# Kernel tuning notes

Hardware: AMD Instinct MI355X
Metric: run time of the kernel (lower is better)

Reference implementation:

```python
import jax, jax.numpy as jnp
import numpy as np

INPUT_DIM = 784
LATENT_DIM = 32
HIDDEN = 256
NUM_PROTO = 25  # 5x5 SOM grid
BATCH = 65536


def setup_inputs() -> dict:
    key = jax.random.key(0)
    ks = jax.random.split(key, 10)
    s = lambda fan_in: 1.0 / np.sqrt(fan_in)
    return {
        "x": jax.random.uniform(ks[0], (BATCH, INPUT_DIM), dtype=jnp.float32),
        # encoder: Linear(784,256) -> ReLU -> Linear(256,32)
        "We1": jax.random.normal(ks[1], (INPUT_DIM, HIDDEN), dtype=jnp.float32) * s(INPUT_DIM),
        "be1": jnp.zeros((HIDDEN,), dtype=jnp.float32),
        "We2": jax.random.normal(ks[2], (HIDDEN, LATENT_DIM), dtype=jnp.float32) * s(HIDDEN),
        "be2": jnp.zeros((LATENT_DIM,), dtype=jnp.float32),
        # decoder: Linear(32,256) -> ReLU -> Linear(256,784) -> Sigmoid
        "Wd1": jax.random.normal(ks[3], (LATENT_DIM, HIDDEN), dtype=jnp.float32) * s(LATENT_DIM),
        "bd1": jnp.zeros((HIDDEN,), dtype=jnp.float32),
        "Wd2": jax.random.normal(ks[4], (HIDDEN, INPUT_DIM), dtype=jnp.float32) * s(HIDDEN),
        "bd2": jnp.zeros((INPUT_DIM,), dtype=jnp.float32),
        # SOM prototypes (torch.randn init)
        "prototypes": jax.random.normal(ks[5], (NUM_PROTO, LATENT_DIM), dtype=jnp.float32),
    }


def reference(x, We1, be1, We2, be2, Wd1, bd1, Wd2, bd2, prototypes):
    # encoder
    h = jax.nn.relu(x @ We1 + be1)          # [B, 256]
    z = h @ We2 + be2                        # [B, 32]
    # SOM layer: cdist -> argmin -> gather winning prototype
    # squared euclidean distance suffices for argmin
    sq_dists = (jnp.sum(z * z, axis=1, keepdims=True)
                - 2.0 * (z @ prototypes.T)
                + jnp.sum(prototypes * prototypes, axis=1))  # [B, 25]
    min_idx = jnp.argmin(sq_dists, axis=1)   # [B]
    som_z = prototypes[min_idx]              # [B, 32]
    # decoder
    hd = jax.nn.relu(som_z @ Wd1 + bd1)      # [B, 256]
    x_recon = jax.nn.sigmoid(hd @ Wd2 + bd2)  # [B, 784]
    return (x_recon, z, som_z)
```

## Files before the change

kernel.cpp:

```cpp
#include <hip/hip_runtime.h>
#include <hip/hip_bf16.h>
#include <math.h>

#define BATCH   65536
#define IN_DIM  784
#define HID     256
#define LAT     32
#define NPROTO  25

typedef short  short8  __attribute__((ext_vector_type(8)));
typedef float  floatx4 __attribute__((ext_vector_type(4)));

__device__ __forceinline__ unsigned short f2bf(float v) {
    __hip_bfloat16 b = __float2bfloat16(v);
    return *reinterpret_cast<unsigned short*>(&b);
}
__device__ __forceinline__ float bf2f(unsigned short u) {
    __hip_bfloat16 b = *reinterpret_cast<__hip_bfloat16*>(&u);
    return __bfloat162float(b);
}
__device__ __forceinline__ void split3(float v, unsigned short& o1,
                                       unsigned short& o2, unsigned short& o3) {
    o1 = f2bf(v); float r1 = v - bf2f(o1);
    o2 = f2bf(r1); float r2 = r1 - bf2f(o2);
    o3 = f2bf(r2);
}

__device__ __forceinline__ floatx4 mm_bf16(short8 a, short8 b, floatx4 c) {
    return __builtin_amdgcn_mfma_f32_16x16x32_bf16(a, b, c, 0, 0, 0);
}

__device__ __forceinline__ void async_copy16(const void* g, void* l) {
    __builtin_amdgcn_global_load_lds(
        (const __attribute__((address_space(1))) unsigned int*)g,
        (__attribute__((address_space(3))) unsigned int*)l, 16, 0, 0);
}

#define BT_BYTES   409600
#define WS_NEEDED  1307200

__global__ __launch_bounds__(256)
void dpsom_prep(const float* __restrict__ We1,
                unsigned short* __restrict__ B1,
                unsigned short* __restrict__ B2,
                unsigned short* __restrict__ B3,
                const float* __restrict__ protos,
                const float* __restrict__ Wd1,
                const float* __restrict__ bd1,
                const float* __restrict__ Wd2,
                const float* __restrict__ bd2,
                float* __restrict__ table)
{
    const int tid = threadIdx.x;
    if (blockIdx.x < 200) {
        int e = (blockIdx.x * 256 + tid) * 4;
        int k = e & 31;
        int n = (e >> 5) & 255;
        int s = e >> 13;
        int cs = (k >> 3) ^ ((n >> 1) & 3);
        int dst = (s * 256 + n) * 32 + cs * 8 + (k & 7);
        ushort4 u1, u2, u3;
        unsigned short a, b, c;
#pragma unroll
        for (int j = 0; j < 4; ++j) {
            int kk = s * 32 + k + j;
            float v = (kk < IN_DIM) ? We1[(size_t)kk * HID + n] : 0.f;
            split3(v, a, b, c);
            ((unsigned short*)&u1)[j] = a;
            ((unsigned short*)&u2)[j] = b;
            ((unsigned short*)&u3)[j] = c;
        }
        *(ushort4*)(B1 + dst) = u1;
        *(ushort4*)(B2 + dst) = u2;
        *(ushort4*)(B3 + dst) = u3;
    } else {
        __shared__ float pr[LAT];
        __shared__ float hd[HID];
        const int p = blockIdx.x - 200;
        if (tid < LAT) pr[tid] = protos[p * LAT + tid];
        __syncthreads();
        float s = bd1[tid];
#pragma unroll
        for (int k = 0; k < LAT; ++k)
            s = fmaf(pr[k], Wd1[k * HID + tid], s);
        hd[tid] = fmaxf(s, 0.f);
        __syncthreads();
        for (int i = tid; i < IN_DIM; i += 256) {
            float o = bd2[i];
            for (int j = 0; j < HID; ++j)
                o = fmaf(hd[j], Wd2[(size_t)j * IN_DIM + i], o);
            table[p * IN_DIM + i] = 1.f / (1.f + expf(-o));
        }
    }
}

__global__ __launch_bounds__(256, 2)
void dpsom_encoder_mfma(const float* __restrict__ x,
                        const unsigned short* __restrict__ B1g,
                        const unsigned short* __restrict__ B2g,
                        const unsigned short* __restrict__ B3g,
                        const float* __restrict__ be1,
                        const float* __restrict__ We2,
                        const float* __restrict__ be2,
                        const float* __restrict__ protos,
                        const float* __restrict__ table,
                        float* __restrict__ z_out,
                        float* __restrict__ somz_out,
                        float* __restrict__ xrec)
{
    __shared__ __align__(16) char smem[61440];
    const int tid  = threadIdx.x;
    const int wave = tid >> 6;
    const int lane = tid & 63;
    const int l15  = lane & 15;
    const int q    = lane >> 4;
    const int sw   = (l15 >> 1) & 3;
    const int row0 = blockIdx.x * 64;

    floatx4 acc[4][4];
#pragma unroll
    for (int i = 0; i < 4; ++i)
#pragma unroll
        for (int j = 0; j < 4; ++j) acc[i][j] = (floatx4)0.f;

    int row_[2], k4_[2], dst_[2];
    const float* xptr[2];
#pragma unroll
    for (int i = 0; i < 2; ++i) {
        int ff = tid + i * 256;
        row_[i] = ff >> 3;
        k4_[i]  = ff & 7;
        int csw = ((k4_[i] >> 1) ^ ((row_[i] >> 1) & 3));
        dst_[i] = row_[i] * 64 + csw * 16 + (k4_[i] & 1) * 8;
        xptr[i] = x + (size_t)(row0 + row_[i]) * IN_DIM + k4_[i] * 4;
    }

    float4 cur[2], nxt[2];
#pragma unroll
    for (int i = 0; i < 2; ++i) cur[i] = *(const float4*)(xptr[i]);

    for (int s = 0; s < 25; ++s) {
        __syncthreads();
        if (s < 24) {
#pragma unroll
            for (int i = 0; i < 2; ++i) {
                nxt[i] = make_float4(0.f, 0.f, 0.f, 0.f);
                if (s + 1 < 24 || k4_[i] < 4)
                    nxt[i] = *(const float4*)(xptr[i] + (s + 1) * 32);
            }
        }
        {
            size_t gbase = (size_t)s * 16384 + (size_t)wave * 4096 + (size_t)lane * 16;
            char* lb = smem + 12288 + wave * 4096 + lane * 16;
#pragma unroll
            for (int i = 0; i < 4; ++i) {
                async_copy16((const char*)B1g + gbase + i * 1024, lb + 0     + i * 1024);
                async_copy16((const char*)B2g + gbase + i * 1024, lb + 16384 + i * 1024);
                async_copy16((const char*)B3g + gbase + i * 1024, lb + 32768 + i * 1024);
            }
        }
#pragma unroll
        for (int i = 0; i < 2; ++i) {
            float4 v = cur[i];
            ushort4 u1, u2, u3;
            unsigned short a, b, c;
            split3(v.x, a, b, c); u1.x = a; u2.x = b; u3.x = c;
            split3(v.y, a, b, c); u1.y = a; u2.y = b; u3.y = c;
            split3(v.z, a, b, c); u1.z = a; u2.z = b; u3.z = c;
            split3(v.w, a, b, c); u1.w = a; u2.w = b; u3.w = c;
            *(ushort4*)(smem + dst_[i])        = u1;
            *(ushort4*)(smem + 4096 + dst_[i]) = u2;
            *(ushort4*)(smem + 8192 + dst_[i]) = u3;
        }
        __syncthreads();

        short8 afr[3][4];
#pragma unroll
        for (int mf = 0; mf < 4; ++mf) {
            int abyte = (16 * mf + l15) * 64 + ((q ^ sw) * 16);
            afr[0][mf] = *(short8*)(smem + abyte);
            afr[1][mf] = *(short8*)(smem + 4096 + abyte);
            afr[2][mf] = *(short8*)(smem + 8192 + abyte);
        }
#pragma unroll
        for (int nf = 0; nf < 4; ++nf) {
            int n = wave * 64 + 16 * nf + l15;
            int bbyte = n * 64 + ((q ^ sw) * 16);
            short8 b1 = *(short8*)(smem + 12288 + bbyte);
            short8 b2 = *(short8*)(smem + 28672 + bbyte);
            short8 b3 = *(short8*)(smem + 45056 + bbyte);
#pragma unroll
            for (int mf = 0; mf < 4; ++mf) {
                floatx4 t = acc[mf][nf];
                t = mm_bf16(afr[0][mf], b1, t);
                t = mm_bf16(afr[0][mf], b2, t);
                t = mm_bf16(afr[1][mf], b1, t);
                t = mm_bf16(afr[1][mf], b2, t);
                t = mm_bf16(afr[0][mf], b3, t);
                t = mm_bf16(afr[2][mf], b1, t);
                acc[mf][nf] = t;
            }
        }
#pragma unroll
        for (int i = 0; i < 2; ++i) cur[i] = nxt[i];
    }

    {
        float bias[4];
#pragma unroll
        for (int nf = 0; nf < 4; ++nf) bias[nf] = be1[wave * 64 + 16 * nf + l15];
#pragma unroll
        for (int mf = 0; mf < 4; ++mf)
#pragma unroll
            for (int nf = 0; nf < 4; ++nf)
#pragma unroll
                for (int r = 0; r < 4; ++r)
                    acc[mf][nf][r] = fmaxf(acc[mf][nf][r] + bias[nf], 0.f);
    }

    float* h_lds = (float*)smem;
    float* z_lds = (float*)(smem + 33280);
    int*  minidx = (int*)(smem + 41728);

    const int jz = tid & 31;
    const int rg = tid >> 5;
    const float bz = be2[jz];

    for (int half = 0; half < 2; ++half) {
        __syncthreads();
#pragma unroll
        for (int mm = 0; mm < 2; ++mm) {
            int mf = 2 * half + mm;
#pragma unroll
            for (int nf = 0; nf < 4; ++nf)
#pragma unroll
                for (int r = 0; r < 4; ++r) {
                    int lr = 16 * mm + 4 * q + r;
                    h_lds[lr * 260 + wave * 64 + 16 * nf + l15] = acc[mf][nf][r];
                }
        }
        __syncthreads();
        float s0 = bz, s1 = bz, s2 = bz, s3 = bz;
        const float* h0p = h_lds + (rg * 4 + 0) * 260;
        const float* h1p = h_lds + (rg * 4 + 1) * 260;
        const float* h2p = h_lds + (rg * 4 + 2) * 260;
        const float* h3p = h_lds + (rg * 4 + 3) * 260;
#pragma unroll 4
        for (int c = 0; c < HID; c += 4) {
            float w0 = We2[(c + 0) * LAT + jz];
            float w1 = We2[(c + 1) * LAT + jz];
            float w2 = We2[(c + 2) * LAT + jz];
            float w3 = We2[(c + 3) * LAT + jz];
            float4 h0 = *(const float4*)(h0p + c);
            float4 h1 = *(const float4*)(h1p + c);
            float4 h2 = *(const float4*)(h2p + c);
            float4 h3 = *(const float4*)(h3p + c);
            s0 = fmaf(h0.x, w0, fmaf(h0.y, w1, fmaf(h0.z, w2, fmaf(h0.w, w3, s0))));
            s1 = fmaf(h1.x, w0, fmaf(h1.y, w1, fmaf(h1.z, w2, fmaf(h1.w, w3, s1))));
            s2 = fmaf(h2.x, w0, fmaf(h2.y, w1, fmaf(h2.z, w2, fmaf(h2.w, w3, s2))));
            s3 = fmaf(h3.x, w0, fmaf(h3.y, w1, fmaf(h3.z, w2, fmaf(h3.w, w3, s3))));
        }
        int rbase = half * 32 + rg * 4;
        z_lds[(rbase + 0) * 33 + jz] = s0;
        z_lds[(rbase + 1) * 33 + jz] = s1;
        z_lds[(rbase + 2) * 33 + jz] = s2;
        z_lds[(rbase + 3) * 33 + jz] = s3;
        z_out[(size_t)(row0 + rbase + 0) * LAT + jz] = s0;
        z_out[(size_t)(row0 + rbase + 1) * LAT + jz] = s1;
        z_out[(size_t)(row0 + rbase + 2) * LAT + jz] = s2;
        z_out[(size_t)(row0 + rbase + 3) * LAT + jz] = s3;
    }
    __syncthreads();

    if (tid < 64) {
        float zr[LAT];
        float zn = 0.f;
#pragma unroll
        for (int j = 0; j < LAT; ++j) {
            zr[j] = z_lds[tid * 33 + j];
            zn = fmaf(zr[j], zr[j], zn);
        }
        float best = 3.4e38f;
        int bp = 0;
        for (int p = 0; p < NPROTO; ++p) {
            float dot = 0.f, pn = 0.f;
#pragma unroll
            for (int j = 0; j < LAT; ++j) {
                float pv = protos[p * LAT + j];
                dot = fmaf(zr[j], pv, dot);
                pn  = fmaf(pv, pv, pn);
            }
            float d = zn - 2.f * dot + pn;
            if (d < best) { best = d; bp = p; }
        }
        minidx[tid] = bp;
    }
    __syncthreads();

#pragma unroll
    for (int m = 0; m < 8; ++m) {
        int r = rg * 8 + m;
        somz_out[(size_t)(row0 + r) * LAT + jz] = protos[minidx[r] * LAT + jz];
    }

    for (int i2 = tid; i2 < 64 * 196; i2 += 256) {
        int row = i2 / 196;
        int c   = i2 - row * 196;
        int idx = minidx[row];
        ((float4*)xrec)[(size_t)(row0 + row) * 196 + c] =
            ((const float4*)table)[idx * 196 + c];
    }
}

#define BMf 64
#define BKf 16
#define HSTRIDE 260
#define ZSTRIDE 33
#define SMEM_FLOATS 10432

__global__ __launch_bounds__(256)
void dpsom_encoder_fp32(const float* __restrict__ x,
                        const float* __restrict__ We1,
                        const float* __restrict__ be1,
                        const float* __restrict__ We2,
                        const float* __restrict__ be2,
                        const float* __restrict__ protos,
                        float* __restrict__ z_out,
                        float* __restrict__ somz_out,
                        int* __restrict__ minidx_out)
{
    __shared__ float smem[SMEM_FLOATS];
    __shared__ int minidx_lds[BMf];
    float* As = smem;
    float* Bs = smem + BKf * BMf;
    float* h_lds = smem;
    float* z_lds = smem + 32 * HSTRIDE;

    const int tid = threadIdx.x;
    const int tx = tid & 31;
    const int ty = tid >> 5;
    const int row0 = blockIdx.x * BMf;

    float acc[8][8];
#pragma unroll
    for (int i = 0; i < 8; ++i)
#pragma unroll
        for (int j = 0; j < 8; ++j) acc[i][j] = 0.f;

    const int ar  = tid >> 2;
    const int akq = tid & 3;

    for (int k0 = 0; k0 < IN_DIM; k0 += BKf) {
        __syncthreads();
        float4 av = *(const float4*)(x + (size_t)(row0 + ar) * IN_DIM + k0 + akq * 4);
        As[(akq * 4 + 0) * BMf + ar] = av.x;
        As[(akq * 4 + 1) * BMf + ar] = av.y;
        As[(akq * 4 + 2) * BMf + ar] = av.z;
        As[(akq * 4 + 3) * BMf + ar] = av.w;
#pragma unroll
        for (int i = 0; i < 4; ++i) {
            int f  = tid + i * 256;
            int bk = f >> 6;
            int bn = (f & 63) << 2;
            *(float4*)(Bs + bk * HID + bn) =
                *(const float4*)(We1 + (size_t)(k0 + bk) * HID + bn);
        }
        __syncthreads();
#pragma unroll
        for (int kk = 0; kk < BKf; ++kk) {
            float4 a0 = *(const float4*)(As + kk * BMf + ty * 8);
            float4 a1 = *(const float4*)(As + kk * BMf + ty * 8 + 4);
            float4 b0 = *(const float4*)(Bs + kk * HID + tx * 8);
            float4 b1 = *(const float4*)(Bs + kk * HID + tx * 8 + 4);
            float a[8] = {a0.x, a0.y, a0.z, a0.w, a1.x, a1.y, a1.z, a1.w};
            float b[8] = {b0.x, b0.y, b0.z, b0.w, b1.x, b1.y, b1.z, b1.w};
#pragma unroll
            for (int i = 0; i < 8; ++i)
#pragma unroll
                for (int j = 0; j < 8; ++j)
                    acc[i][j] = fmaf(a[i], b[j], acc[i][j]);
        }
    }
    {
        float bias[8];
#pragma unroll
        for (int j = 0; j < 8; ++j) bias[j] = be1[tx * 8 + j];
#pragma unroll
        for (int i = 0; i < 8; ++i)
#pragma unroll
            for (int j = 0; j < 8; ++j)
                acc[i][j] = fmaxf(acc[i][j] + bias[j], 0.f);
    }
    const int jz = tid & 31;
    const int rg = tid >> 5;
    const float bz = be2[jz];
    for (int half = 0; half < 2; ++half) {
        __syncthreads();
        if ((ty >> 2) == half) {
            int rb = (ty & 3) * 8;
#pragma unroll
            for (int i = 0; i < 8; ++i) {
                *(float4*)(h_lds + (rb + i) * HSTRIDE + tx * 8) =
                    make_float4(acc[i][0], acc[i][1], acc[i][2], acc[i][3]);
                *(float4*)(h_lds + (rb + i) * HSTRIDE + tx * 8 + 4) =
                    make_float4(acc[i][4], acc[i][5], acc[i][6], acc[i][7]);
            }
        }
        __syncthreads();
        float s0 = bz, s1 = bz, s2 = bz, s3 = bz;
        const float* h0p = h_lds + (rg * 4 + 0) * HSTRIDE;
        const float* h1p = h_lds + (rg * 4 + 1) * HSTRIDE;
        const float* h2p = h_lds + (rg * 4 + 2) * HSTRIDE;
        const float* h3p = h_lds + (rg * 4 + 3) * HSTRIDE;
#pragma unroll 4
        for (int c = 0; c < HID; c += 4) {
            float w0 = We2[(c + 0) * LAT + jz];
            float w1 = We2[(c + 1) * LAT + jz];
            float w2 = We2[(c + 2) * LAT + jz];
            float w3 = We2[(c + 3) * LAT + jz];
            float4 h0 = *(const float4*)(h0p + c);
            float4 h1 = *(const float4*)(h1p + c);
            float4 h2 = *(const float4*)(h2p + c);
            float4 h3 = *(const float4*)(h3p + c);
            s0 = fmaf(h0.x, w0, fmaf(h0.y, w1, fmaf(h0.z, w2, fmaf(h0.w, w3, s0))));
            s1 = fmaf(h1.x, w0, fmaf(h1.y, w1, fmaf(h1.z, w2, fmaf(h1.w, w3, s1))));
            s2 = fmaf(h2.x, w0, fmaf(h2.y, w1, fmaf(h2.z, w2, fmaf(h2.w, w3, s2))));
            s3 = fmaf(h3.x, w0, fmaf(h3.y, w1, fmaf(h3.z, w2, fmaf(h3.w, w3, s3))));
        }
        int rbase = half * 32 + rg * 4;
        z_lds[(rbase + 0) * ZSTRIDE + jz] = s0;
        z_lds[(rbase + 1) * ZSTRIDE + jz] = s1;
        z_lds[(rbase + 2) * ZSTRIDE + jz] = s2;
        z_lds[(rbase + 3) * ZSTRIDE + jz] = s3;
        z_out[(size_t)(row0 + rbase + 0) * LAT + jz] = s0;
        z_out[(size_t)(row0 + rbase + 1) * LAT + jz] = s1;
        z_out[(size_t)(row0 + rbase + 2) * LAT + jz] = s2;
        z_out[(size_t)(row0 + rbase + 3) * LAT + jz] = s3;
    }
    __syncthreads();
    if (tid < BMf) {
        float zr[LAT];
        float zn = 0.f;
#pragma unroll
        for (int j = 0; j < LAT; ++j) {
            zr[j] = z_lds[tid * ZSTRIDE + j];
            zn = fmaf(zr[j], zr[j], zn);
        }
        float best = 3.4e38f;
        int bp = 0;
        for (int p = 0; p < NPROTO; ++p) {
            float dot = 0.f, pn = 0.f;
#pragma unroll
            for (int j = 0; j < LAT; ++j) {
                float pv = protos[p * LAT + j];
                dot = fmaf(zr[j], pv, dot);
                pn  = fmaf(pv, pv, pn);
            }
            float d = zn - 2.f * dot + pn;
            if (d < best) { best = d; bp = p; }
        }
        minidx_out[row0 + tid] = bp;
        minidx_lds[tid] = bp;
    }
    __syncthreads();
#pragma unroll
    for (int m = 0; m < 8; ++m) {
        int r = rg * 8 + m;
        somz_out[(size_t)(row0 + r) * LAT + jz] = protos[minidx_lds[r] * LAT + jz];
    }
}

__global__ __launch_bounds__(256)
void dpsom_dectab(const float* __restrict__ protos,
                  const float* __restrict__ Wd1,
                  const float* __restrict__ bd1,
                  const float* __restrict__ Wd2,
                  const float* __restrict__ bd2,
                  float* __restrict__ table)
{
    __shared__ float pr[LAT];
    __shared__ float hd[HID];
    const int p = blockIdx.x;
    const int tid = threadIdx.x;
    if (tid < LAT) pr[tid] = protos[p * LAT + tid];
    __syncthreads();
    float s = bd1[tid];
#pragma unroll
    for (int k = 0; k < LAT; ++k)
        s = fmaf(pr[k], Wd1[k * HID + tid], s);
    hd[tid] = fmaxf(s, 0.f);
    __syncthreads();
    for (int i = tid; i < IN_DIM; i += 256) {
        float o = bd2[i];
        for (int j = 0; j < HID; ++j)
            o = fmaf(hd[j], Wd2[(size_t)j * IN_DIM + i], o);
        table[p * IN_DIM + i] = 1.f / (1.f + expf(-o));
    }
}

__global__ __launch_bounds__(256)
void dpsom_gather(const float4* __restrict__ table,
                  const int* __restrict__ minidx,
                  float4* __restrict__ xrec)
{
    const int f = blockIdx.x * 256 + threadIdx.x;
    const int row = f / 196;
    const int c4  = f - row * 196;
    const int idx = minidx[row];
    xrec[f] = table[idx * 196 + c4];
}

extern "C" void kernel_launch(void* const* d_in, const int* in_sizes, int n_in,
                              void* d_out, int out_size, void* d_ws, size_t ws_size,
                              hipStream_t stream)
{
    const float* x    = (const float*)d_in[0];
    const float* We1  = (const float*)d_in[1];
    const float* be1  = (const float*)d_in[2];
    const float* We2  = (const float*)d_in[3];
    const float* be2  = (const float*)d_in[4];
    const float* Wd1  = (const float*)d_in[5];
    const float* bd1  = (const float*)d_in[6];
    const float* Wd2  = (const float*)d_in[7];
    const float* bd2  = (const float*)d_in[8];
    const float* prot = (const float*)d_in[9];

    float* out   = (float*)d_out;
    float* xrec  = out;
    float* z_out = out + (size_t)BATCH * IN_DIM;
    float* somz  = z_out + (size_t)BATCH * LAT;

    if (ws_size >= WS_NEEDED) {
        unsigned short* B1 = (unsigned short*)d_ws;
        unsigned short* B2 = (unsigned short*)((char*)d_ws + BT_BYTES);
        unsigned short* B3 = (unsigned short*)((char*)d_ws + 2 * BT_BYTES);
        float* table = (float*)((char*)d_ws + 3 * BT_BYTES);

        hipLaunchKernelGGL(dpsom_prep, dim3(225), dim3(256), 0, stream,
                           We1, B1, B2, B3, prot, Wd1, bd1, Wd2, bd2, table);
        hipLaunchKernelGGL(dpsom_encoder_mfma, dim3(BATCH / 64), dim3(256), 0, stream,
                           x, B1, B2, B3, be1, We2, be2, prot, table,
                           z_out, somz, xrec);
    } else {
        int*   minidx = (int*)d_ws;
        float* table  = (float*)((char*)d_ws + (size_t)BATCH * 4);
        hipLaunchKernelGGL(dpsom_encoder_fp32, dim3(BATCH / BMf), dim3(256), 0, stream,
                           x, We1, be1, We2, be2, prot, z_out, somz, minidx);
        hipLaunchKernelGGL(dpsom_dectab, dim3(NPROTO), dim3(256), 0, stream,
                           prot, Wd1, bd1, Wd2, bd2, table);
        hipLaunchKernelGGL(dpsom_gather, dim3((BATCH * (IN_DIM / 4)) / 256), dim3(256), 0, stream,
                           (const float4*)table, minidx, (float4*)xrec);
    }
}
```

Measured before the change: 547.4 us.

## Load encoder weight fragments directly from global and double-buffer x tiles in LDS

Removes the async global-to-LDS staging of the three bf16 weight splits: each wave now loads its B fragments straight from global memory into registers, and the prep kernel drops the LDS swizzle. The x tile is double-buffered in LDS, so each step needs one barrier instead of two, and the split/store for the next step runs after the MFMAs. LDS use falls from about 60KB to about 41KB, which may allow more resident blocks. The cost is that every block re-reads the weights from global/L2 with non-coalesced per-lane 16-byte loads, and these loads are issued just before the MFMAs that use them, which could stall.

```diff
diff --git a/kernel.cpp b/kernel.cpp
--- a/kernel.cpp
+++ b/kernel.cpp
@@ -28,12 +28,6 @@
 
 __device__ __forceinline__ floatx4 mm_bf16(short8 a, short8 b, floatx4 c) {
     return __builtin_amdgcn_mfma_f32_16x16x32_bf16(a, b, c, 0, 0, 0);
-}
-
-__device__ __forceinline__ void async_copy16(const void* g, void* l) {
-    __builtin_amdgcn_global_load_lds(
-        (const __attribute__((address_space(1))) unsigned int*)g,
-        (__attribute__((address_space(3))) unsigned int*)l, 16, 0, 0);
 }
 
 #define BT_BYTES   409600
@@ -57,8 +51,7 @@
         int k = e & 31;
         int n = (e >> 5) & 255;
         int s = e >> 13;
-        int cs = (k >> 3) ^ ((n >> 1) & 3);
-        int dst = (s * 256 + n) * 32 + cs * 8 + (k & 7);
+        int dst = (s * 256 + n) * 32 + k;
         ushort4 u1, u2, u3;
         unsigned short a, b, c;
 #pragma unroll
@@ -108,7 +101,7 @@
                         float* __restrict__ somz_out,
                         float* __restrict__ xrec)
 {
-    __shared__ __align__(16) char smem[61440];
+    __shared__ __align__(16) char smem[41984];
     const int tid  = threadIdx.x;
     const int wave = tid >> 6;
     const int lane = tid & 63;
@@ -123,86 +116,96 @@
 #pragma unroll
         for (int j = 0; j < 4; ++j) acc[i][j] = (floatx4)0.f;
 
-    int row_[2], k4_[2], dst_[2];
+    int k4_[2], dst_[2];
     const float* xptr[2];
 #pragma unroll
     for (int i = 0; i < 2; ++i) {
         int ff = tid + i * 256;
-        row_[i] = ff >> 3;
+        int row = ff >> 3;
         k4_[i]  = ff & 7;
-        int csw = ((k4_[i] >> 1) ^ ((row_[i] >> 1) & 3));
-        dst_[i] = row_[i] * 64 + csw * 16 + (k4_[i] & 1) * 8;
-        xptr[i] = x + (size_t)(row0 + row_[i]) * IN_DIM + k4_[i] * 4;
-    }
-
-    float4 cur[2], nxt[2];
-#pragma unroll
-    for (int i = 0; i < 2; ++i) cur[i] = *(const float4*)(xptr[i]);
+        int csw = ((k4_[i] >> 1) ^ ((row >> 1) & 3));
+        dst_[i] = row * 64 + csw * 16 + (k4_[i] & 1) * 8;
+        xptr[i] = x + (size_t)(row0 + row) * IN_DIM + k4_[i] * 4;
+    }
+
+#pragma unroll
+    for (int i = 0; i < 2; ++i) {
+        float4 v = *(const float4*)(xptr[i]);
+        ushort4 u1, u2, u3;
+        unsigned short a, b, c;
+        split3(v.x, a, b, c); u1.x = a; u2.x = b; u3.x = c;
+        split3(v.y, a, b, c); u1.y = a; u2.y = b; u3.y = c;
+        split3(v.z, a, b, c); u1.z = a; u2.z = b; u3.z = c;
+        split3(v.w, a, b, c); u1.w = a; u2.w = b; u3.w = c;
+        *(ushort4*)(smem + dst_[i])        = u1;
+        *(ushort4*)(smem + 4096 + dst_[i]) = u2;
+        *(ushort4*)(smem + 8192 + dst_[i]) = u3;
+    }
+    __syncthreads();
 
     for (int s = 0; s < 25; ++s) {
-        __syncthreads();
+        const int cb = (s & 1) * 12288;
+        const int nb = ((s + 1) & 1) * 12288;
+
+        short8 bf1[4], bf2[4], bf3[4];
+#pragma unroll
+        for (int nf = 0; nf < 4; ++nf) {
+            size_t off = ((size_t)(s * 256 + wave * 64 + nf * 16 + l15)) * 32 + q * 8;
+            bf1[nf] = *(const short8*)(B1g + off);
+            bf2[nf] = *(const short8*)(B2g + off);
+            bf3[nf] = *(const short8*)(B3g + off);
+        }
+
+        float4 xv[2];
         if (s < 24) {
 #pragma unroll
             for (int i = 0; i < 2; ++i) {
-                nxt[i] = make_float4(0.f, 0.f, 0.f, 0.f);
+                xv[i] = make_float4(0.f, 0.f, 0.f, 0.f);
                 if (s + 1 < 24 || k4_[i] < 4)
-                    nxt[i] = *(const float4*)(xptr[i] + (s + 1) * 32);
+                    xv[i] = *(const float4*)(xptr[i] + (s + 1) * 32);
             }
         }
-        {
-            size_t gbase = (size_t)s * 16384 + (size_t)wave * 4096 + (size_t)lane * 16;
-            char* lb = smem + 12288 + wave * 4096 + lane * 16;
-#pragma unroll
-            for (int i = 0; i < 4; ++i) {
-                async_copy16((const char*)B1g + gbase + i * 1024, lb + 0     + i * 1024);
-                async_copy16((const char*)B2g + gbase + i * 1024, lb + 16384 + i * 1024);
-                async_copy16((const char*)B3g + gbase + i * 1024, lb + 32768 + i * 1024);
-            }
-        }
-#pragma unroll
-        for (int i = 0; i < 2; ++i) {
-            float4 v = cur[i];
-            ushort4 u1, u2, u3;
-            unsigned short a, b, c;
-            split3(v.x, a, b, c); u1.x = a; u2.x = b; u3.x = c;
-            split3(v.y, a, b, c); u1.y = a; u2.y = b; u3.y = c;
-            split3(v.z, a, b, c); u1.z = a; u2.z = b; u3.z = c;
-            split3(v.w, a, b, c); u1.w = a; u2.w = b; u3.w = c;
-            *(ushort4*)(smem + dst_[i])        = u1;
-            *(ushort4*)(smem + 4096 + dst_[i]) = u2;
-            *(ushort4*)(smem + 8192 + dst_[i]) = u3;
-        }
-        __syncthreads();
-
-        short8 afr[3][4];
+
+        short8 af1[4], af2[4], af3[4];
 #pragma unroll
         for (int mf = 0; mf < 4; ++mf) {
             int abyte = (16 * mf + l15) * 64 + ((q ^ sw) * 16);
-            afr[0][mf] = *(short8*)(smem + abyte);
-            afr[1][mf] = *(short8*)(smem + 4096 + abyte);
-            afr[2][mf] = *(short8*)(smem + 8192 + abyte);
-        }
+            af1[mf] = *(short8*)(smem + cb + abyte);
+            af2[mf] = *(short8*)(smem + cb + 4096 + abyte);
+            af3[mf] = *(short8*)(smem + cb + 8192 + abyte);
+        }
+
 #pragma unroll
         for (int nf = 0; nf < 4; ++nf) {
-            int n = wave * 64 + 16 * nf + l15;
-            int bbyte = n * 64 + ((q ^ sw) * 16);
-            short8 b1 = *(short8*)(smem + 12288 + bbyte);
-            short8 b2 = *(short8*)(smem + 28672 + bbyte);
-            short8 b3 = *(short8*)(smem + 45056 + bbyte);
 #pragma unroll
             for (int mf = 0; mf < 4; ++mf) {
                 floatx4 t = acc[mf][nf];
-                t = mm_bf16(afr[0][mf], b1, t);
-                t = mm_bf16(afr[0][mf], b2, t);
-                t = mm_bf16(afr[1][mf], b1, t);
-                t = mm_bf16(afr[1][mf], b2, t);
-                t = mm_bf16(afr[0][mf], b3, t);
-                t = mm_bf16(afr[2][mf], b1, t);
+                t = mm_bf16(af1[mf], bf1[nf], t);
+                t = mm_bf16(af1[mf], bf2[nf], t);
+                t = mm_bf16(af2[mf], bf1[nf], t);
+                t = mm_bf16(af2[mf], bf2[nf], t);
+                t = mm_bf16(af1[mf], bf3[nf], t);
+                t = mm_bf16(af3[mf], bf1[nf], t);
                 acc[mf][nf] = t;
             }
         }
-#pragma unroll
-        for (int i = 0; i < 2; ++i) cur[i] = nxt[i];
+
+        if (s < 24) {
+#pragma unroll
+            for (int i = 0; i < 2; ++i) {
+                float4 v = xv[i];
+                ushort4 u1, u2, u3;
+                unsigned short a, b, c;
+                split3(v.x, a, b, c); u1.x = a; u2.x = b; u3.x = c;
+                split3(v.y, a, b, c); u1.y = a; u2.y = b; u3.y = c;
+                split3(v.z, a, b, c); u1.z = a; u2.z = b; u3.z = c;
+                split3(v.w, a, b, c); u1.w = a; u2.w = b; u3.w = c;
+                *(ushort4*)(smem + nb + dst_[i])        = u1;
+                *(ushort4*)(smem + nb + 4096 + dst_[i]) = u2;
+                *(ushort4*)(smem + nb + 8192 + dst_[i]) = u3;
+            }
+        }
+        __syncthreads();
     }
 
     {
```

Result: faster. 536.3 us (-2.0%).
